# Optimization experiments

Measured on AMD Instinct MI355X. Metric: run time of the kernel, lower is better.

Reference implementation:

```python
import jax, jax.numpy as jnp
import numpy as np

N_NODES = 50000
IN_CH, HID, OUT_CH = 512, 128, 64
N_EDGES = 800000


def gcn_conv(x, edge_index, W, b, num_nodes):
    # PyG GCNConv: add self-loops, symmetric deg^{-1/2} normalization,
    # linear transform then scatter-add aggregation at target nodes.
    row, col = edge_index[0], edge_index[1]
    loop = jnp.arange(num_nodes, dtype=row.dtype)
    rows = jnp.concatenate([row, loop])  # sources
    cols = jnp.concatenate([col, loop])  # targets
    deg = jax.ops.segment_sum(jnp.ones_like(cols, dtype=x.dtype), cols, num_segments=num_nodes)
    dinv = jnp.where(deg > 0, jax.lax.rsqrt(deg), 0.0)
    norm = dinv[rows] * dinv[cols]  # [E+N]
    h = x @ W  # [N, out]
    msg = norm[:, None] * h[rows]  # gather + scale
    out = jax.ops.segment_sum(msg, cols, num_segments=num_nodes)
    return out + b


def setup_inputs() -> dict:
    key = jax.random.key(0)
    k = jax.random.split(key, 8)
    x = jax.random.normal(k[0], (N_NODES, IN_CH), dtype=jnp.float32)
    pos_edge_index = jax.random.randint(k[1], (2, N_EDGES), 0, N_NODES, dtype=jnp.int64 if jax.config.jax_enable_x64 else jnp.int32)
    neg_edge_index = jax.random.randint(k[2], (2, N_EDGES), 0, N_NODES, dtype=pos_edge_index.dtype)
    # Glorot-ish init for weights, zeros for bias (PyG default)
    W1 = jax.random.normal(k[3], (IN_CH, HID), dtype=jnp.float32) * (1.0 / np.sqrt(IN_CH))
    b1 = jnp.zeros((HID,), dtype=jnp.float32)
    W2 = jax.random.normal(k[4], (HID, OUT_CH), dtype=jnp.float32) * (1.0 / np.sqrt(HID))
    b2 = jnp.zeros((OUT_CH,), dtype=jnp.float32)
    return {"x": x, "pos_edge_index": pos_edge_index, "neg_edge_index": neg_edge_index,
            "W1": W1, "b1": b1, "W2": W2, "b2": b2}


def reference(x, pos_edge_index, neg_edge_index, W1, b1, W2, b2):
    n = x.shape[0]
    h = gcn_conv(x, pos_edge_index, W1, b1, n)
    h = jax.nn.relu(h)
    z = gcn_conv(h, pos_edge_index, W2, b2, n)  # encode
    edge_index = jnp.concatenate([pos_edge_index, neg_edge_index], axis=-1)
    # decode: per-edge dot product of endpoint embeddings
    logits = jnp.sum(z[edge_index[0]] * z[edge_index[1]], axis=-1)
    return logits
```

## Files before the change

### kernel.cpp

```cpp
#include <hip/hip_runtime.h>

#define WAVE 64
#define CAP 64

typedef __bf16 v8bf __attribute__((ext_vector_type(8)));
typedef __bf16 v4bf __attribute__((ext_vector_type(4)));
typedef __bf16 v2bf __attribute__((ext_vector_type(2)));
typedef float f32x4 __attribute__((ext_vector_type(4)));

__global__ __launch_bounds__(256) void prep_kernel(const float* __restrict__ W1,
                                                   const float* __restrict__ W2,
                                                   __bf16* __restrict__ Wt1hi,
                                                   __bf16* __restrict__ Wt1lo,
                                                   __bf16* __restrict__ Wt2hi,
                                                   __bf16* __restrict__ Wt2lo) {
    int b = blockIdx.x;
    int tid = threadIdx.x;
    if (b < 256) {
        int idx = b * 256 + tid;
        int k = idx >> 7, n = idx & 127;
        float v = W1[idx];
        __bf16 h = (__bf16)v;
        Wt1hi[n * 512 + k] = h;
        Wt1lo[n * 512 + k] = (__bf16)(v - (float)h);
    } else {
        int idx = (b - 256) * 256 + tid;
        int k = idx >> 6, n = idx & 63;
        float v = W2[idx];
        __bf16 h = (__bf16)v;
        Wt2hi[n * 128 + k] = h;
        Wt2lo[n * 128 + k] = (__bf16)(v - (float)h);
    }
}

template <int NC, int KK, bool OBF16, bool FILL>
__global__ __launch_bounds__(256, 3) void gemm_fill_kernel(
    const float* __restrict__ A, const __bf16* __restrict__ Bhi,
    const __bf16* __restrict__ Blo, void* __restrict__ Cout, int M, int NG,
    const int* __restrict__ ei, int E, int* __restrict__ cursor,
    int* __restrict__ srcs) {
    constexpr int BK = 32;
    constexpr int LD = 40;
    constexpr int NT = NC / 16;
    constexpr int CPT = (NC * 4) / 256;

    __shared__ __bf16 sAhi[128][LD];
    __shared__ __bf16 sAlo[128][LD];
    __shared__ __bf16 sBhi[NC][LD];
    __shared__ __bf16 sBlo[NC][LD];

    const int tid = threadIdx.x;

    if (FILL && blockIdx.x >= NG) {
        int bb = (blockIdx.x - NG) * 512;
#pragma unroll
        for (int j = 0; j < 2; ++j) {
            int e = bb + tid + j * 256;
            if (e < E) {
                int dst = ei[E + e];
                int p = atomicAdd(&cursor[dst], 1);
                if (p < CAP) srcs[(size_t)dst * CAP + p] = ei[e];
            }
        }
        return;
    }

    const int lane = tid & 63;
    const int wv = tid >> 6;
    const int ln15 = lane & 15;
    const int quad = lane >> 4;
    const int rowBase = blockIdx.x * 128;

    const int sr = tid >> 1;
    const int kh = (tid & 1) * 16;
    const int gr = rowBase + sr;
    const bool aval = gr < M;
    const float* aBase = A + (size_t)gr * KK + kh;

    int bcol[CPT], bg[CPT];
#pragma unroll
    for (int c = 0; c < CPT; ++c) {
        int chunk = tid * CPT + c;
        bcol[c] = chunk >> 2;
        bg[c] = chunk & 3;
    }

    f32x4 acc[2][NT];
#pragma unroll
    for (int rt = 0; rt < 2; ++rt)
#pragma unroll
        for (int t = 0; t < NT; ++t) acc[rt][t] = (f32x4){0.f, 0.f, 0.f, 0.f};

    float4 aR[4];
    v8bf bhR[CPT], blR[CPT];

    auto loadTiles = [&](int k0) {
        if (aval) {
#pragma unroll
            for (int q = 0; q < 4; ++q) aR[q] = *(const float4*)(aBase + k0 + q * 4);
        } else {
#pragma unroll
            for (int q = 0; q < 4; ++q) aR[q] = make_float4(0.f, 0.f, 0.f, 0.f);
        }
#pragma unroll
        for (int c = 0; c < CPT; ++c) {
            bhR[c] = *(const v8bf*)(Bhi + (size_t)bcol[c] * KK + k0 + bg[c] * 8);
            blR[c] = *(const v8bf*)(Blo + (size_t)bcol[c] * KK + k0 + bg[c] * 8);
        }
    };

    loadTiles(0);

    for (int k0 = 0; k0 < KK; k0 += BK) {
        float fv[16];
#pragma unroll
        for (int q = 0; q < 4; ++q) {
            fv[q * 4 + 0] = aR[q].x; fv[q * 4 + 1] = aR[q].y;
            fv[q * 4 + 2] = aR[q].z; fv[q * 4 + 3] = aR[q].w;
        }
#pragma unroll
        for (int g = 0; g < 2; ++g) {
            v8bf hv, lv;
#pragma unroll
            for (int j = 0; j < 8; ++j) {
                float v = fv[g * 8 + j];
                __bf16 h = (__bf16)v;
                hv[j] = h;
                lv[j] = (__bf16)(v - (float)h);
            }
            *(v8bf*)&sAhi[sr][kh + g * 8] = hv;
            *(v8bf*)&sAlo[sr][kh + g * 8] = lv;
        }
#pragma unroll
        for (int c = 0; c < CPT; ++c) {
            *(v8bf*)&sBhi[bcol[c]][bg[c] * 8] = bhR[c];
            *(v8bf*)&sBlo[bcol[c]][bg[c] * 8] = blR[c];
        }
        __syncthreads();

        if (k0 + BK < KK) loadTiles(k0 + BK);

        v8bf ah[2], al[2];
#pragma unroll
        for (int rt = 0; rt < 2; ++rt) {
            int r = wv * 32 + rt * 16 + ln15;
            ah[rt] = *(const v8bf*)&sAhi[r][quad * 8];
            al[rt] = *(const v8bf*)&sAlo[r][quad * 8];
        }
#pragma unroll
        for (int t = 0; t < NT; ++t) {
            v8bf bh = *(const v8bf*)&sBhi[t * 16 + ln15][quad * 8];
            v8bf bl = *(const v8bf*)&sBlo[t * 16 + ln15][quad * 8];
#pragma unroll
            for (int rt = 0; rt < 2; ++rt) {
                acc[rt][t] = __builtin_amdgcn_mfma_f32_16x16x32_bf16(ah[rt], bh, acc[rt][t], 0, 0, 0);
                acc[rt][t] = __builtin_amdgcn_mfma_f32_16x16x32_bf16(al[rt], bh, acc[rt][t], 0, 0, 0);
                acc[rt][t] = __builtin_amdgcn_mfma_f32_16x16x32_bf16(ah[rt], bl, acc[rt][t], 0, 0, 0);
            }
        }
        __syncthreads();
    }

#pragma unroll
    for (int rt = 0; rt < 2; ++rt) {
#pragma unroll
        for (int r = 0; r < 4; ++r) {
            int grow = rowBase + wv * 32 + rt * 16 + quad * 4 + r;
            if (grow < M) {
#pragma unroll
                for (int t = 0; t < NT; ++t) {
                    float v = acc[rt][t][r];
                    if (OBF16)
                        ((__bf16*)Cout)[(size_t)grow * NC + t * 16 + ln15] = (__bf16)v;
                    else
                        ((float*)Cout)[(size_t)grow * NC + t * 16 + ln15] = v;
                }
            }
        }
    }
}

template <int F, bool RELU, bool BF16OUT>
__global__ __launch_bounds__(256) void gather_agg_bf16(const __bf16* __restrict__ hs,
                                                       const int* __restrict__ counts,
                                                       const int* __restrict__ srcs,
                                                       const float* __restrict__ bias,
                                                       void* __restrict__ outp, int N) {
    int node = blockIdx.x * 4 + (int)(threadIdx.x >> 6);
    if (node >= N) return;
    int lane = threadIdx.x & 63;
    int cnt = counts[node];
    if (cnt > CAP) cnt = CAP;
    int beg = node * CAP;
    int end = beg + cnt;
    float dn = rsqrtf((float)cnt + 1.0f);

    if constexpr (F == 128) {
        int col = 2 * lane;
        float a0, a1;
        {
            v2bf s = *(const v2bf*)&hs[(size_t)node * F + col];
            a0 = dn * (float)s[0];
            a1 = dn * (float)s[1];
        }
        int e = beg;
        for (; e + 4 <= end; e += 4) {
            int s0 = srcs[e], s1 = srcs[e + 1], s2 = srcs[e + 2], s3 = srcs[e + 3];
            float d0 = rsqrtf((float)counts[s0] + 1.0f);
            float d1 = rsqrtf((float)counts[s1] + 1.0f);
            float d2 = rsqrtf((float)counts[s2] + 1.0f);
            float d3 = rsqrtf((float)counts[s3] + 1.0f);
            v2bf r0 = *(const v2bf*)&hs[(size_t)s0 * F + col];
            v2bf r1 = *(const v2bf*)&hs[(size_t)s1 * F + col];
            v2bf r2 = *(const v2bf*)&hs[(size_t)s2 * F + col];
            v2bf r3 = *(const v2bf*)&hs[(size_t)s3 * F + col];
            a0 += d0 * (float)r0[0] + d1 * (float)r1[0] + d2 * (float)r2[0] + d3 * (float)r3[0];
            a1 += d0 * (float)r0[1] + d1 * (float)r1[1] + d2 * (float)r2[1] + d3 * (float)r3[1];
        }
        for (; e < end; ++e) {
            int s0 = srcs[e];
            float d0 = rsqrtf((float)counts[s0] + 1.0f);
            v2bf r0 = *(const v2bf*)&hs[(size_t)s0 * F + col];
            a0 += d0 * (float)r0[0];
            a1 += d0 * (float)r0[1];
        }
        float2 bv = *(const float2*)&bias[col];
        float v0 = dn * a0 + bv.x;
        float v1 = dn * a1 + bv.y;
        if (RELU) {
            v0 = fmaxf(v0, 0.f);
            v1 = fmaxf(v1, 0.f);
        }
        if (BF16OUT) {
            v2bf o;
            o[0] = (__bf16)v0;
            o[1] = (__bf16)v1;
            *(v2bf*)&((__bf16*)outp)[(size_t)node * F + col] = o;
        } else {
            *(float2*)&((float*)outp)[(size_t)node * F + col] = make_float2(v0, v1);
        }
    } else {
        int q = lane >> 4;
        int sl = lane & 15;
        int col = sl * 4;
        float a0 = 0.f, a1 = 0.f, a2 = 0.f, a3 = 0.f;
        if (q == 0) {
            v4bf s = *(const v4bf*)&hs[(size_t)node * F + col];
            a0 = dn * (float)s[0]; a1 = dn * (float)s[1];
            a2 = dn * (float)s[2]; a3 = dn * (float)s[3];
        }
        int e = beg + q;
        for (; e + 4 < end; e += 8) {
            int s0 = srcs[e], s1 = srcs[e + 4];
            float d0 = rsqrtf((float)counts[s0] + 1.0f);
            float d1 = rsqrtf((float)counts[s1] + 1.0f);
            v4bf r0 = *(const v4bf*)&hs[(size_t)s0 * F + col];
            v4bf r1 = *(const v4bf*)&hs[(size_t)s1 * F + col];
            a0 += d0 * (float)r0[0] + d1 * (float)r1[0];
            a1 += d0 * (float)r0[1] + d1 * (float)r1[1];
            a2 += d0 * (float)r0[2] + d1 * (float)r1[2];
            a3 += d0 * (float)r0[3] + d1 * (float)r1[3];
        }
        if (e < end) {
            int s0 = srcs[e];
            float d0 = rsqrtf((float)counts[s0] + 1.0f);
            v4bf r0 = *(const v4bf*)&hs[(size_t)s0 * F + col];
            a0 += d0 * (float)r0[0]; a1 += d0 * (float)r0[1];
            a2 += d0 * (float)r0[2]; a3 += d0 * (float)r0[3];
        }
        a0 += __shfl_xor(a0, 16); a0 += __shfl_xor(a0, 32);
        a1 += __shfl_xor(a1, 16); a1 += __shfl_xor(a1, 32);
        a2 += __shfl_xor(a2, 16); a2 += __shfl_xor(a2, 32);
        a3 += __shfl_xor(a3, 16); a3 += __shfl_xor(a3, 32);
        if (q == 0) {
            float4 bv = *(const float4*)&bias[col];
            float v0 = dn * a0 + bv.x;
            float v1 = dn * a1 + bv.y;
            float v2 = dn * a2 + bv.z;
            float v3 = dn * a3 + bv.w;
            if (RELU) {
                v0 = fmaxf(v0, 0.f); v1 = fmaxf(v1, 0.f);
                v2 = fmaxf(v2, 0.f); v3 = fmaxf(v3, 0.f);
            }
            if (BF16OUT) {
                v4bf o;
                o[0] = (__bf16)v0; o[1] = (__bf16)v1;
                o[2] = (__bf16)v2; o[3] = (__bf16)v3;
                *(v4bf*)&((__bf16*)outp)[(size_t)node * F + col] = o;
            } else {
                *(float4*)&((float*)outp)[(size_t)node * F + col] =
                    make_float4(v0, v1, v2, v3);
            }
        }
    }
}

__global__ __launch_bounds__(256) void decode_bf16_kernel(const __bf16* __restrict__ z,
                                                          const int* __restrict__ pos,
                                                          const int* __restrict__ neg, int E,
                                                          float* __restrict__ out) {
    int tid = blockIdx.x * blockDim.x + threadIdx.x;
    int g = tid >> 2;
    int l = tid & 3;
    int total = 2 * E;
    if (g >= total) return;
    int src, dst;
    if (g < E) {
        src = pos[g];
        dst = pos[E + g];
    } else {
        int e = g - E;
        src = neg[e];
        dst = neg[E + e];
    }
    const __bf16* zs = z + (size_t)src * 64 + l * 16;
    const __bf16* zd = z + (size_t)dst * 64 + l * 16;
    v8bf a0 = *(const v8bf*)zs;
    v8bf a1 = *(const v8bf*)(zs + 8);
    v8bf b0 = *(const v8bf*)zd;
    v8bf b1 = *(const v8bf*)(zd + 8);
    float p = 0.f;
#pragma unroll
    for (int j = 0; j < 8; ++j) p += (float)a0[j] * (float)b0[j] + (float)a1[j] * (float)b1[j];
    p += __shfl_xor(p, 1);
    p += __shfl_xor(p, 2);
    if (l == 0) out[g] = p;
}

extern "C" void kernel_launch(void* const* d_in, const int* in_sizes, int n_in, void* d_out,
                              int out_size, void* d_ws, size_t ws_size, hipStream_t stream) {
    const float* x = (const float*)d_in[0];
    const int* pos_ei = (const int*)d_in[1];
    const int* neg_ei = (const int*)d_in[2];
    const float* W1 = (const float*)d_in[3];
    const float* b1 = (const float*)d_in[4];
    const float* W2 = (const float*)d_in[5];
    const float* b2 = (const float*)d_in[6];
    float* out = (float*)d_out;

    const int IN = 512, HID = 128, OUT = 64;
    const int N = in_sizes[0] / IN;
    const int E = in_sizes[1] / 2;

    size_t nAlign = ((size_t)N + 255) & ~(size_t)255;
    float* p = (float*)d_ws;
    float* h1 = p; p += (size_t)N * HID;
    __bf16* hs1 = (__bf16*)p; p += (size_t)N * HID / 2;
    __bf16* hs2 = (__bf16*)p; p += (size_t)N * OUT / 2;
    __bf16* zbf = (__bf16*)p; p += (size_t)N * OUT / 2;
    int* cursor = (int*)p; p += nAlign;
    int* srcs = (int*)p; p += (size_t)N * CAP;
    __bf16* Wt1hi = (__bf16*)p; p += (size_t)IN * HID / 2;
    __bf16* Wt1lo = (__bf16*)p; p += (size_t)IN * HID / 2;
    __bf16* Wt2hi = (__bf16*)p; p += (size_t)HID * OUT / 2;
    __bf16* Wt2lo = (__bf16*)p; p += (size_t)HID * OUT / 2;

    const int NG = (N + 127) / 128;
    const int NF = (E + 511) / 512;

    hipMemsetAsync(cursor, 0, (size_t)N * sizeof(int), stream);
    prep_kernel<<<288, 256, 0, stream>>>(W1, W2, Wt1hi, Wt1lo, Wt2hi, Wt2lo);

    gemm_fill_kernel<128, 512, true, true><<<NG + NF, 256, 0, stream>>>(
        x, Wt1hi, Wt1lo, hs1, N, NG, pos_ei, E, cursor, srcs);
    gather_agg_bf16<128, true, false>
        <<<(N + 3) / 4, 256, 0, stream>>>(hs1, cursor, srcs, b1, h1, N);

    gemm_fill_kernel<64, 128, true, false><<<NG, 256, 0, stream>>>(
        h1, Wt2hi, Wt2lo, hs2, N, NG, nullptr, 0, nullptr, nullptr);
    gather_agg_bf16<64, false, true>
        <<<(N + 3) / 4, 256, 0, stream>>>(hs2, cursor, srcs, b2, zbf, N);

    decode_bf16_kernel<<<((size_t)2 * E * 4 + 255) / 256, 256, 0, stream>>>(
        zbf, pos_ei, neg_ei, E, out);
}
```

Before: 312.9 us.

## Stage GEMM tiles via async global-to-LDS loads with double buffering and swizzle

Replaces the register-staged A/B tile loads with direct global_load_lds copies into double-buffered, XOR-swizzled shared memory. The fp32 A tile is kept in LDS and split into bf16 hi/lo parts after the LDS read instead of before the store. The goal is to overlap the next tile's loads with the current MFMAs and to cut VGPR staging and bank conflicts. In exchange, LDS use roughly doubles and the occupancy hint drops from 3 to 2 blocks per SM, and each wave now repeats the hi/lo conversion on its own fragments.

```diff
diff --git a/kernel.cpp b/kernel.cpp
--- a/kernel.cpp
+++ b/kernel.cpp
@@ -7,6 +7,11 @@
 typedef __bf16 v4bf __attribute__((ext_vector_type(4)));
 typedef __bf16 v2bf __attribute__((ext_vector_type(2)));
 typedef float f32x4 __attribute__((ext_vector_type(4)));
+
+__device__ __forceinline__ void async16(void* lds, const void* g) {
+    __builtin_amdgcn_global_load_lds((const __attribute__((address_space(1))) void*)g,
+                                     (__attribute__((address_space(3))) void*)lds, 16, 0, 0);
+}
 
 __global__ __launch_bounds__(256) void prep_kernel(const float* __restrict__ W1,
                                                    const float* __restrict__ W2,
@@ -34,20 +39,18 @@
 }
 
 template <int NC, int KK, bool OBF16, bool FILL>
-__global__ __launch_bounds__(256, 3) void gemm_fill_kernel(
+__global__ __launch_bounds__(256, 2) void gemm_fill_kernel(
     const float* __restrict__ A, const __bf16* __restrict__ Bhi,
     const __bf16* __restrict__ Blo, void* __restrict__ Cout, int M, int NG,
     const int* __restrict__ ei, int E, int* __restrict__ cursor,
     int* __restrict__ srcs) {
     constexpr int BK = 32;
-    constexpr int LD = 40;
     constexpr int NT = NC / 16;
-    constexpr int CPT = (NC * 4) / 256;
-
-    __shared__ __bf16 sAhi[128][LD];
-    __shared__ __bf16 sAlo[128][LD];
-    __shared__ __bf16 sBhi[NC][LD];
-    __shared__ __bf16 sBlo[NC][LD];
+    constexpr int NIT = KK / BK;
+    constexpr int CHB = NC / 16;
+
+    __shared__ float sA[2][128 * 32];
+    __shared__ __bf16 sB[2][2][NC * 32];
 
     const int tid = threadIdx.x;
 
@@ -71,19 +74,27 @@
     const int quad = lane >> 4;
     const int rowBase = blockIdx.x * 128;
 
-    const int sr = tid >> 1;
-    const int kh = (tid & 1) * 16;
-    const int gr = rowBase + sr;
-    const bool aval = gr < M;
-    const float* aBase = A + (size_t)gr * KK + kh;
-
-    int bcol[CPT], bg[CPT];
-#pragma unroll
-    for (int c = 0; c < CPT; ++c) {
-        int chunk = tid * CPT + c;
-        bcol[c] = chunk >> 2;
-        bg[c] = chunk & 3;
-    }
+    auto stageA = [&](int buf, int k0) {
+#pragma unroll
+        for (int i = 0; i < 4; ++i) {
+            int c = wv + i * 4;
+            int row = c * 8 + (lane >> 3);
+            int p = lane & 7;
+            int grow = rowBase + row;
+            if (grow > M - 1) grow = M - 1;
+            int gcol = k0 + ((p ^ (row & 7)) << 2);
+            async16(&sA[buf][c * 256], A + (size_t)grow * KK + gcol);
+        }
+    };
+    auto stageB = [&](int buf, int k0) {
+        for (int i = wv; i < CHB; i += 4) {
+            int row = i * 16 + (lane >> 2);
+            int p = lane & 3;
+            int gk = k0 + ((p ^ ((row >> 1) & 3)) << 3);
+            async16(&sB[buf][0][i * 512], Bhi + (size_t)row * KK + gk);
+            async16(&sB[buf][1][i * 512], Blo + (size_t)row * KK + gk);
+        }
+    };
 
     f32x4 acc[2][NT];
 #pragma unroll
@@ -91,66 +102,40 @@
 #pragma unroll
         for (int t = 0; t < NT; ++t) acc[rt][t] = (f32x4){0.f, 0.f, 0.f, 0.f};
 
-    float4 aR[4];
-    v8bf bhR[CPT], blR[CPT];
-
-    auto loadTiles = [&](int k0) {
-        if (aval) {
-#pragma unroll
-            for (int q = 0; q < 4; ++q) aR[q] = *(const float4*)(aBase + k0 + q * 4);
-        } else {
-#pragma unroll
-            for (int q = 0; q < 4; ++q) aR[q] = make_float4(0.f, 0.f, 0.f, 0.f);
-        }
-#pragma unroll
-        for (int c = 0; c < CPT; ++c) {
-            bhR[c] = *(const v8bf*)(Bhi + (size_t)bcol[c] * KK + k0 + bg[c] * 8);
-            blR[c] = *(const v8bf*)(Blo + (size_t)bcol[c] * KK + k0 + bg[c] * 8);
-        }
-    };
-
-    loadTiles(0);
-
-    for (int k0 = 0; k0 < KK; k0 += BK) {
-        float fv[16];
-#pragma unroll
-        for (int q = 0; q < 4; ++q) {
-            fv[q * 4 + 0] = aR[q].x; fv[q * 4 + 1] = aR[q].y;
-            fv[q * 4 + 2] = aR[q].z; fv[q * 4 + 3] = aR[q].w;
-        }
-#pragma unroll
-        for (int g = 0; g < 2; ++g) {
-            v8bf hv, lv;
+    stageA(0, 0);
+    stageB(0, 0);
+    __syncthreads();
+
+    int cur = 0;
+    for (int it = 0; it < NIT; ++it) {
+        if (it + 1 < NIT) {
+            stageA(cur ^ 1, (it + 1) * BK);
+            stageB(cur ^ 1, (it + 1) * BK);
+        }
+
+        v8bf ah[2], al[2];
+#pragma unroll
+        for (int rt = 0; rt < 2; ++rt) {
+            int row = wv * 32 + rt * 16 + ln15;
+            int sw = row & 7;
+            const float* base = &sA[cur][row * 32];
+            f32x4 u = *(const f32x4*)(base + (((2 * quad) ^ sw) << 2));
+            f32x4 v = *(const f32x4*)(base + (((2 * quad + 1) ^ sw) << 2));
+            float f[8] = {u.x, u.y, u.z, u.w, v.x, v.y, v.z, v.w};
 #pragma unroll
             for (int j = 0; j < 8; ++j) {
-                float v = fv[g * 8 + j];
-                __bf16 h = (__bf16)v;
-                hv[j] = h;
-                lv[j] = (__bf16)(v - (float)h);
-            }
-            *(v8bf*)&sAhi[sr][kh + g * 8] = hv;
-            *(v8bf*)&sAlo[sr][kh + g * 8] = lv;
-        }
-#pragma unroll
-        for (int c = 0; c < CPT; ++c) {
-            *(v8bf*)&sBhi[bcol[c]][bg[c] * 8] = bhR[c];
-            *(v8bf*)&sBlo[bcol[c]][bg[c] * 8] = blR[c];
-        }
-        __syncthreads();
-
-        if (k0 + BK < KK) loadTiles(k0 + BK);
-
-        v8bf ah[2], al[2];
-#pragma unroll
-        for (int rt = 0; rt < 2; ++rt) {
-            int r = wv * 32 + rt * 16 + ln15;
-            ah[rt] = *(const v8bf*)&sAhi[r][quad * 8];
-            al[rt] = *(const v8bf*)&sAlo[r][quad * 8];
-        }
+                __bf16 h = (__bf16)f[j];
+                ah[rt][j] = h;
+                al[rt][j] = (__bf16)(f[j] - (float)h);
+            }
+        }
+
 #pragma unroll
         for (int t = 0; t < NT; ++t) {
-            v8bf bh = *(const v8bf*)&sBhi[t * 16 + ln15][quad * 8];
-            v8bf bl = *(const v8bf*)&sBlo[t * 16 + ln15][quad * 8];
+            int row = t * 16 + ln15;
+            int sw = (row >> 1) & 3;
+            v8bf bh = *(const v8bf*)&sB[cur][0][row * 32 + ((quad ^ sw) << 3)];
+            v8bf bl = *(const v8bf*)&sB[cur][1][row * 32 + ((quad ^ sw) << 3)];
 #pragma unroll
             for (int rt = 0; rt < 2; ++rt) {
                 acc[rt][t] = __builtin_amdgcn_mfma_f32_16x16x32_bf16(ah[rt], bh, acc[rt][t], 0, 0, 0);
@@ -158,7 +143,9 @@
                 acc[rt][t] = __builtin_amdgcn_mfma_f32_16x16x32_bf16(ah[rt], bl, acc[rt][t], 0, 0, 0);
             }
         }
+
         __syncthreads();
+        cur ^= 1;
     }
 
 #pragma unroll
```

Result: slower. 325.0 us (+3.9%).

## Fuse layer-1 aggregation with layer-2 GEMM via shared-memory tile and MFMA

Applied to the files above, without the earlier changes.

Replaces the separate layer-1 gather/aggregate kernel and the second GEMM with one kernel. Each block aggregates 16 nodes into a shared-memory fp32 tile, then multiplies that tile by W2 using split-bf16 MFMA. W2 is stored in a k-chunked layout to suit the fused kernel. This removes the fp32 h1 round trip through global memory and one launch. The cost is a block-wide sync between the latency-bound gather phase and a small GEMM phase, and only 16 nodes per block.

```diff
diff --git a/kernel.cpp b/kernel.cpp
--- a/kernel.cpp
+++ b/kernel.cpp
@@ -7,6 +7,16 @@
 typedef __bf16 v4bf __attribute__((ext_vector_type(4)));
 typedef __bf16 v2bf __attribute__((ext_vector_type(2)));
 typedef float f32x4 __attribute__((ext_vector_type(4)));
+
+__device__ __forceinline__ void cvt8(const f32x4& u, const f32x4& v, v8bf& h, v8bf& l) {
+    float f[8] = {u.x, u.y, u.z, u.w, v.x, v.y, v.z, v.w};
+#pragma unroll
+    for (int j = 0; j < 8; ++j) {
+        __bf16 hh = (__bf16)f[j];
+        h[j] = hh;
+        l[j] = (__bf16)(f[j] - (float)hh);
+    }
+}
 
 __global__ __launch_bounds__(256) void prep_kernel(const float* __restrict__ W1,
                                                    const float* __restrict__ W2,
@@ -28,8 +38,9 @@
         int k = idx >> 6, n = idx & 63;
         float v = W2[idx];
         __bf16 h = (__bf16)v;
-        Wt2hi[n * 128 + k] = h;
-        Wt2lo[n * 128 + k] = (__bf16)(v - (float)h);
+        int o = (k >> 5) * (64 * 32) + n * 32 + (k & 31);
+        Wt2hi[o] = h;
+        Wt2lo[o] = (__bf16)(v - (float)h);
     }
 }
 
@@ -177,6 +188,89 @@
                 }
             }
         }
+    }
+}
+
+__global__ __launch_bounds__(256) void gather1_gemm2_kernel(
+    const __bf16* __restrict__ hs, const int* __restrict__ counts,
+    const int* __restrict__ srcs, const float* __restrict__ bias,
+    const __bf16* __restrict__ W2hi, const __bf16* __restrict__ W2lo,
+    __bf16* __restrict__ hs2, int N) {
+    constexpr int LDO = 132;
+    __shared__ float out1[16 * LDO];
+
+    const int tid = threadIdx.x;
+    const int lane = tid & 63;
+    const int wv = tid >> 6;
+    const int base = blockIdx.x * 16;
+
+    for (int i = 0; i < 4; ++i) {
+        int slot = wv * 4 + i;
+        int node = base + slot;
+        float v0 = 0.f, v1 = 0.f;
+        int col = 2 * lane;
+        if (node < N) {
+            int cnt = counts[node];
+            if (cnt > CAP) cnt = CAP;
+            int beg = node * CAP;
+            int end = beg + cnt;
+            float dn = rsqrtf((float)cnt + 1.0f);
+            float a0, a1;
+            {
+                v2bf s = *(const v2bf*)&hs[(size_t)node * 128 + col];
+                a0 = dn * (float)s[0];
+                a1 = dn * (float)s[1];
+            }
+            int e = beg;
+            for (; e + 4 <= end; e += 4) {
+                int s0 = srcs[e], s1 = srcs[e + 1], s2 = srcs[e + 2], s3 = srcs[e + 3];
+                float d0 = rsqrtf((float)counts[s0] + 1.0f);
+                float d1 = rsqrtf((float)counts[s1] + 1.0f);
+                float d2 = rsqrtf((float)counts[s2] + 1.0f);
+                float d3 = rsqrtf((float)counts[s3] + 1.0f);
+                v2bf r0 = *(const v2bf*)&hs[(size_t)s0 * 128 + col];
+                v2bf r1 = *(const v2bf*)&hs[(size_t)s1 * 128 + col];
+                v2bf r2 = *(const v2bf*)&hs[(size_t)s2 * 128 + col];
+                v2bf r3 = *(const v2bf*)&hs[(size_t)s3 * 128 + col];
+                a0 += d0 * (float)r0[0] + d1 * (float)r1[0] + d2 * (float)r2[0] + d3 * (float)r3[0];
+                a1 += d0 * (float)r0[1] + d1 * (float)r1[1] + d2 * (float)r2[1] + d3 * (float)r3[1];
+            }
+            for (; e < end; ++e) {
+                int s0 = srcs[e];
+                float d0 = rsqrtf((float)counts[s0] + 1.0f);
+                v2bf r0 = *(const v2bf*)&hs[(size_t)s0 * 128 + col];
+                a0 += d0 * (float)r0[0];
+                a1 += d0 * (float)r0[1];
+            }
+            float2 bv = *(const float2*)&bias[col];
+            v0 = fmaxf(dn * a0 + bv.x, 0.f);
+            v1 = fmaxf(dn * a1 + bv.y, 0.f);
+        }
+        *(float2*)&out1[slot * LDO + col] = make_float2(v0, v1);
+    }
+    __syncthreads();
+
+    const int ln15 = lane & 15;
+    const int quad = lane >> 4;
+    f32x4 acc = (f32x4){0.f, 0.f, 0.f, 0.f};
+#pragma unroll
+    for (int kc = 0; kc < 4; ++kc) {
+        const float* ap = &out1[ln15 * LDO + kc * 32 + quad * 8];
+        f32x4 u = *(const f32x4*)(ap);
+        f32x4 v = *(const f32x4*)(ap + 4);
+        v8bf ah, al;
+        cvt8(u, v, ah, al);
+        size_t bo = (size_t)kc * (64 * 32) + (wv * 16 + ln15) * 32 + quad * 8;
+        v8bf bh = *(const v8bf*)(W2hi + bo);
+        v8bf bl = *(const v8bf*)(W2lo + bo);
+        acc = __builtin_amdgcn_mfma_f32_16x16x32_bf16(ah, bh, acc, 0, 0, 0);
+        acc = __builtin_amdgcn_mfma_f32_16x16x32_bf16(al, bh, acc, 0, 0, 0);
+        acc = __builtin_amdgcn_mfma_f32_16x16x32_bf16(ah, bl, acc, 0, 0, 0);
+    }
+#pragma unroll
+    for (int r = 0; r < 4; ++r) {
+        int node = base + quad * 4 + r;
+        if (node < N) hs2[(size_t)node * 64 + wv * 16 + ln15] = (__bf16)acc[r];
     }
 }
 
@@ -195,102 +289,56 @@
     int end = beg + cnt;
     float dn = rsqrtf((float)cnt + 1.0f);
 
-    if constexpr (F == 128) {
-        int col = 2 * lane;
-        float a0, a1;
-        {
-            v2bf s = *(const v2bf*)&hs[(size_t)node * F + col];
-            a0 = dn * (float)s[0];
-            a1 = dn * (float)s[1];
-        }
-        int e = beg;
-        for (; e + 4 <= end; e += 4) {
-            int s0 = srcs[e], s1 = srcs[e + 1], s2 = srcs[e + 2], s3 = srcs[e + 3];
-            float d0 = rsqrtf((float)counts[s0] + 1.0f);
-            float d1 = rsqrtf((float)counts[s1] + 1.0f);
-            float d2 = rsqrtf((float)counts[s2] + 1.0f);
-            float d3 = rsqrtf((float)counts[s3] + 1.0f);
-            v2bf r0 = *(const v2bf*)&hs[(size_t)s0 * F + col];
-            v2bf r1 = *(const v2bf*)&hs[(size_t)s1 * F + col];
-            v2bf r2 = *(const v2bf*)&hs[(size_t)s2 * F + col];
-            v2bf r3 = *(const v2bf*)&hs[(size_t)s3 * F + col];
-            a0 += d0 * (float)r0[0] + d1 * (float)r1[0] + d2 * (float)r2[0] + d3 * (float)r3[0];
-            a1 += d0 * (float)r0[1] + d1 * (float)r1[1] + d2 * (float)r2[1] + d3 * (float)r3[1];
-        }
-        for (; e < end; ++e) {
-            int s0 = srcs[e];
-            float d0 = rsqrtf((float)counts[s0] + 1.0f);
-            v2bf r0 = *(const v2bf*)&hs[(size_t)s0 * F + col];
-            a0 += d0 * (float)r0[0];
-            a1 += d0 * (float)r0[1];
-        }
-        float2 bv = *(const float2*)&bias[col];
+    int q = lane >> 4;
+    int sl = lane & 15;
+    int col = sl * 4;
+    float a0 = 0.f, a1 = 0.f, a2 = 0.f, a3 = 0.f;
+    if (q == 0) {
+        v4bf s = *(const v4bf*)&hs[(size_t)node * F + col];
+        a0 = dn * (float)s[0]; a1 = dn * (float)s[1];
+        a2 = dn * (float)s[2]; a3 = dn * (float)s[3];
+    }
+    int e = beg + q;
+    for (; e + 4 < end; e += 8) {
+        int s0 = srcs[e], s1 = srcs[e + 4];
+        float d0 = rsqrtf((float)counts[s0] + 1.0f);
+        float d1 = rsqrtf((float)counts[s1] + 1.0f);
+        v4bf r0 = *(const v4bf*)&hs[(size_t)s0 * F + col];
+        v4bf r1 = *(const v4bf*)&hs[(size_t)s1 * F + col];
+        a0 += d0 * (float)r0[0] + d1 * (float)r1[0];
+        a1 += d0 * (float)r0[1] + d1 * (float)r1[1];
+        a2 += d0 * (float)r0[2] + d1 * (float)r1[2];
+        a3 += d0 * (float)r0[3] + d1 * (float)r1[3];
+    }
+    if (e < end) {
+        int s0 = srcs[e];
+        float d0 = rsqrtf((float)counts[s0] + 1.0f);
+        v4bf r0 = *(const v4bf*)&hs[(size_t)s0 * F + col];
+        a0 += d0 * (float)r0[0]; a1 += d0 * (float)r0[1];
+        a2 += d0 * (float)r0[2]; a3 += d0 * (float)r0[3];
+    }
+    a0 += __shfl_xor(a0, 16); a0 += __shfl_xor(a0, 32);
+    a1 += __shfl_xor(a1, 16); a1 += __shfl_xor(a1, 32);
+    a2 += __shfl_xor(a2, 16); a2 += __shfl_xor(a2, 32);
+    a3 += __shfl_xor(a3, 16); a3 += __shfl_xor(a3, 32);
+    if (q == 0) {
+        float4 bv = *(const float4*)&bias[col];
         float v0 = dn * a0 + bv.x;
         float v1 = dn * a1 + bv.y;
+        float v2 = dn * a2 + bv.z;
+        float v3 = dn * a3 + bv.w;
         if (RELU) {
-            v0 = fmaxf(v0, 0.f);
-            v1 = fmaxf(v1, 0.f);
+            v0 = fmaxf(v0, 0.f); v1 = fmaxf(v1, 0.f);
+            v2 = fmaxf(v2, 0.f); v3 = fmaxf(v3, 0.f);
         }
         if (BF16OUT) {
-            v2bf o;
-            o[0] = (__bf16)v0;
-            o[1] = (__bf16)v1;
-            *(v2bf*)&((__bf16*)outp)[(size_t)node * F + col] = o;
+            v4bf o;
+            o[0] = (__bf16)v0; o[1] = (__bf16)v1;
+            o[2] = (__bf16)v2; o[3] = (__bf16)v3;
+            *(v4bf*)&((__bf16*)outp)[(size_t)node * F + col] = o;
         } else {
-            *(float2*)&((float*)outp)[(size_t)node * F + col] = make_float2(v0, v1);
-        }
-    } else {
-        int q = lane >> 4;
-        int sl = lane & 15;
-        int col = sl * 4;
-        float a0 = 0.f, a1 = 0.f, a2 = 0.f, a3 = 0.f;
-        if (q == 0) {
-            v4bf s = *(const v4bf*)&hs[(size_t)node * F + col];
-            a0 = dn * (float)s[0]; a1 = dn * (float)s[1];
-            a2 = dn * (float)s[2]; a3 = dn * (float)s[3];
-        }
-        int e = beg + q;
-        for (; e + 4 < end; e += 8) {
-            int s0 = srcs[e], s1 = srcs[e + 4];
-            float d0 = rsqrtf((float)counts[s0] + 1.0f);
-            float d1 = rsqrtf((float)counts[s1] + 1.0f);
-            v4bf r0 = *(const v4bf*)&hs[(size_t)s0 * F + col];
-            v4bf r1 = *(const v4bf*)&hs[(size_t)s1 * F + col];
-            a0 += d0 * (float)r0[0] + d1 * (float)r1[0];
-            a1 += d0 * (float)r0[1] + d1 * (float)r1[1];
-            a2 += d0 * (float)r0[2] + d1 * (float)r1[2];
-            a3 += d0 * (float)r0[3] + d1 * (float)r1[3];
-        }
-        if (e < end) {
-            int s0 = srcs[e];
-            float d0 = rsqrtf((float)counts[s0] + 1.0f);
-            v4bf r0 = *(const v4bf*)&hs[(size_t)s0 * F + col];
-            a0 += d0 * (float)r0[0]; a1 += d0 * (float)r0[1];
-            a2 += d0 * (float)r0[2]; a3 += d0 * (float)r0[3];
-        }
-        a0 += __shfl_xor(a0, 16); a0 += __shfl_xor(a0, 32);
-        a1 += __shfl_xor(a1, 16); a1 += __shfl_xor(a1, 32);
-        a2 += __shfl_xor(a2, 16); a2 += __shfl_xor(a2, 32);
-        a3 += __shfl_xor(a3, 16); a3 += __shfl_xor(a3, 32);
-        if (q == 0) {
-            float4 bv = *(const float4*)&bias[col];
-            float v0 = dn * a0 + bv.x;
-            float v1 = dn * a1 + bv.y;
-            float v2 = dn * a2 + bv.z;
-            float v3 = dn * a3 + bv.w;
-            if (RELU) {
-                v0 = fmaxf(v0, 0.f); v1 = fmaxf(v1, 0.f);
-                v2 = fmaxf(v2, 0.f); v3 = fmaxf(v3, 0.f);
-            }
-            if (BF16OUT) {
-                v4bf o;
-                o[0] = (__bf16)v0; o[1] = (__bf16)v1;
-                o[2] = (__bf16)v2; o[3] = (__bf16)v3;
-                *(v4bf*)&((__bf16*)outp)[(size_t)node * F + col] = o;
-            } else {
-                *(float4*)&((float*)outp)[(size_t)node * F + col] =
-                    make_float4(v0, v1, v2, v3);
-            }
+            *(float4*)&((float*)outp)[(size_t)node * F + col] =
+                make_float4(v0, v1, v2, v3);
         }
     }
 }
@@ -344,7 +392,6 @@
 
     size_t nAlign = ((size_t)N + 255) & ~(size_t)255;
     float* p = (float*)d_ws;
-    float* h1 = p; p += (size_t)N * HID;
     __bf16* hs1 = (__bf16*)p; p += (size_t)N * HID / 2;
     __bf16* hs2 = (__bf16*)p; p += (size_t)N * OUT / 2;
     __bf16* zbf = (__bf16*)p; p += (size_t)N * OUT / 2;
@@ -363,11 +410,10 @@
 
     gemm_fill_kernel<128, 512, true, true><<<NG + NF, 256, 0, stream>>>(
         x, Wt1hi, Wt1lo, hs1, N, NG, pos_ei, E, cursor, srcs);
-    gather_agg_bf16<128, true, false>
-        <<<(N + 3) / 4, 256, 0, stream>>>(hs1, cursor, srcs, b1, h1, N);
-
-    gemm_fill_kernel<64, 128, true, false><<<NG, 256, 0, stream>>>(
-        h1, Wt2hi, Wt2lo, hs2, N, NG, nullptr, 0, nullptr, nullptr);
+
+    gather1_gemm2_kernel<<<(N + 15) / 16, 256, 0, stream>>>(
+        hs1, cursor, srcs, b1, Wt2hi, Wt2lo, hs2, N);
+
     gather_agg_bf16<64, false, true>
         <<<(N + 3) / 4, 256, 0, stream>>>(hs2, cursor, srcs, b2, zbf, N);
 
```

Result: no change. 315.6 us (+0.9%).
